# Kernel optimization log

Hardware: AMD Instinct MI355X
Metric: run time of the kernel (lower is better)

The kernel has to match this reference:

```python
import jax, jax.numpy as jnp
import numpy as np

HEADS = 12
NUM_IMS = 1
SCALE = 1.0


def _layernorm(x, g, b, eps=1e-5):
    m = jnp.mean(x, axis=-1, keepdims=True)
    v = jnp.var(x, axis=-1, keepdims=True)
    return (x - m) / jnp.sqrt(v + eps) * g + b


def _mha(q, k, v):
    # q: [B, Nq, C], k/v: [B, Nk, C]; multi-head softmax attention
    B, Nq, C = q.shape
    d = C // HEADS
    qh = q.reshape(B, Nq, HEADS, d)
    kh = k.reshape(B, k.shape[1], HEADS, d)
    vh = v.reshape(B, v.shape[1], HEADS, d)
    sim = jnp.einsum('bihd,bjhd->bhij', qh, kh) * (d ** -0.5)
    w = jax.nn.softmax(sim, axis=-1)
    out = jnp.einsum('bhij,bjhd->bihd', w, vh)
    return out.reshape(B, Nq, C)


def _forward(hidden_states, encoder_hidden_states, ln1_g, ln1_b, ln2_g, ln2_b,
             sa_wq, sa_wk, sa_wv, sa_wo, sa_wo_b, ff_ln_g, ff_ln_b, ff_w1, ff_w2,
             alpha_attn, alpha_dense, ca_wq, ca_wk, ca_wv, ca_wo, ca_wo_b):
    B, N, C = hidden_states.shape
    end_pos = encoder_hidden_states.shape[1] - 16 * NUM_IMS
    text = encoder_hidden_states[:, :end_pos]   # [B, Lt, C]
    face = encoder_hidden_states[:, end_pos:]   # [B, 16, C]

    x = hidden_states
    # gated self-attention over visual tokens + face tokens
    x_ln = _layernorm(x, ln1_g, ln1_b)
    face_ln = _layernorm(face, ln1_g, ln1_b)
    comb = jnp.concatenate([x_ln, face_ln], axis=1)  # [B, N+16, C]
    attn_out = _mha(comb @ sa_wq, comb @ sa_wk, comb @ sa_wv) @ sa_wo + sa_wo_b
    attn_out = attn_out[:, :N]
    x = x + SCALE * jnp.tanh(alpha_attn) * attn_out

    # gated GEGLU feed-forward (norm2 outside, FF has its own LayerNorm)
    h = _layernorm(x, ln2_g, ln2_b)
    h = _layernorm(h, ff_ln_g, ff_ln_b)
    h = h @ ff_w1                                 # [B, N, 2*inner]
    a, gate = jnp.split(h, 2, axis=-1)
    h = (a * jax.nn.gelu(gate, approximate=False)) @ ff_w2
    x = x + SCALE * jnp.tanh(alpha_dense) * h

    residual = x
    # cross attention against text tokens (diffusers Attention, residual_connection=True)
    out = _mha(x @ ca_wq, text @ ca_wk, text @ ca_wv) @ ca_wo + ca_wo_b
    return out + residual


def setup_inputs() -> dict:
    key = jax.random.key(0)
    ks = jax.random.split(key, 16)
    B, N, C, L, INNER = 2, 1024, 768, 77 + 16 * NUM_IMS, 3072
    W = 0.02
    return {
        'hidden_states': jax.random.normal(ks[0], (B, N, C), jnp.float32),
        'encoder_hidden_states': jax.random.normal(ks[1], (B, L, C), jnp.float32),
        'ln1_g': jnp.ones((C,), jnp.float32),
        'ln1_b': jnp.zeros((C,), jnp.float32),
        'ln2_g': jnp.ones((C,), jnp.float32),
        'ln2_b': jnp.zeros((C,), jnp.float32),
        'sa_wq': jax.random.normal(ks[2], (C, C), jnp.float32) * W,
        'sa_wk': jax.random.normal(ks[3], (C, C), jnp.float32) * W,
        'sa_wv': jax.random.normal(ks[4], (C, C), jnp.float32) * W,
        'sa_wo': jax.random.normal(ks[5], (C, C), jnp.float32) * W,
        'sa_wo_b': jnp.zeros((C,), jnp.float32),
        'ff_ln_g': jnp.ones((C,), jnp.float32),
        'ff_ln_b': jnp.zeros((C,), jnp.float32),
        'ff_w1': jax.random.normal(ks[6], (C, 2 * INNER), jnp.float32) * W,
        'ff_w2': jax.random.normal(ks[7], (INNER, C), jnp.float32) * W,
        'alpha_attn': jnp.float32(0.5),
        'alpha_dense': jnp.float32(0.5),
        'ca_wq': jax.random.normal(ks[8], (C, C), jnp.float32) * W,
        'ca_wk': jax.random.normal(ks[9], (C, C), jnp.float32) * W,
        'ca_wv': jax.random.normal(ks[10], (C, C), jnp.float32) * W,
        'ca_wo': jax.random.normal(ks[11], (C, C), jnp.float32) * W,
        'ca_wo_b': jnp.zeros((C,), jnp.float32),
    }


def reference(hidden_states, encoder_hidden_states, ln1_g, ln1_b, ln2_g, ln2_b,
              sa_wq, sa_wk, sa_wv, sa_wo, sa_wo_b, ff_ln_g, ff_ln_b, ff_w1, ff_w2,
              alpha_attn, alpha_dense, ca_wq, ca_wk, ca_wv, ca_wo, ca_wo_b):
    return _forward(hidden_states, encoder_hidden_states, ln1_g, ln1_b, ln2_g, ln2_b,
                    sa_wq, sa_wk, sa_wv, sa_wo, sa_wo_b, ff_ln_g, ff_ln_b, ff_w1, ff_w2,
                    alpha_attn, alpha_dense, ca_wq, ca_wk, ca_wv, ca_wo, ca_wo_b)
```

## Files before the change

### kernel.cpp

```cpp
#include <hip/hip_runtime.h>
#include <hip/hip_bf16.h>
#include <math.h>


#define C_DIM 768
#define B_DIM 2
#define N_DIM 1024
#define NC_DIM 1040
#define L_DIM 93
#define TEXT_LEN 77
#define INNER 3072
#define MNX 1572864

typedef unsigned short ushort_t;
typedef __bf16 bf16x8 __attribute__((ext_vector_type(8)));
typedef float f32x4 __attribute__((ext_vector_type(4)));

__device__ __forceinline__ ushort_t f2b(float f) {
  __hip_bfloat16 h = __float2bfloat16(f);
  return *(ushort_t*)&h;
}
__device__ __forceinline__ float b2f(ushort_t u) {
  __hip_bfloat16 h = *(__hip_bfloat16*)&u;
  return __bfloat162float(h);
}

__device__ __forceinline__ void g2lds16(const void* g, void* l) {
  __builtin_amdgcn_global_load_lds(
      (const __attribute__((address_space(1))) unsigned int*)g,
      (__attribute__((address_space(3))) unsigned int*)l, 16, 0, 0);
}

#define WX1    0u
#define WX2    6291456u
#define WQKV   12582912u
#define WBB1   22167552u
#define WG     47333376u
#define WS1    59916288u
#define WTEXT  63062016u
#define WATT2  63298560u
#define WWQKV  66444288u
#define WWO    69983232u
#define WW1    71162880u
#define WW2    80600064u
#define WCAWQ  85318656u
#define WCAKV  86498304u
#define WCAWO  88857600u
#define WVT1   90037248u
#define WVT2   93379584u
#define WOPART WBB1
#define WLBUF  WG
#define WATTN  (WG + 524288u)
#define WPART  WBB1

__device__ __forceinline__ float block_sum(float v, float* sh) {
#pragma unroll
  for (int o = 32; o > 0; o >>= 1) v += __shfl_down(v, o);
  int lane = threadIdx.x & 63, w = threadIdx.x >> 6;
  if (lane == 0) sh[w] = v;
  __syncthreads();
  float r = sh[0] + sh[1] + sh[2] + sh[3];
  __syncthreads();
  return r;
}

struct WtDesc {
  const float* src[10];
  ushort_t*    dst[10];
  int K[10];
  int N[10];
  int tilesX[10];
  int ileave[10];
  int start[11];
};

__global__ __launch_bounds__(256)
void wtrans_batched(WtDesc d) {
  __shared__ float tile[64][65];
  int bid = blockIdx.x;
  int j = 0;
  while (j < 9 && bid >= d.start[j + 1]) ++j;
  int ti = bid - d.start[j];
  int K = d.K[j], N = d.N[j];
  int n0 = (ti % d.tilesX[j]) * 64, k0 = (ti / d.tilesX[j]) * 64;
  const float* in = d.src[j];
  ushort_t* out = d.dst[j];
  int il = d.ileave[j];
  int t = threadIdx.x;
#pragma unroll
  for (int p = 0; p < 16; ++p) {
    int idx = t + p * 256;
    int r = idx >> 6, c = idx & 63;
    tile[r][c] = in[(size_t)(k0 + r) * N + n0 + c];
  }
  __syncthreads();
#pragma unroll
  for (int p = 0; p < 16; ++p) {
    int idx = t + p * 256;
    int r = idx >> 6, c = idx & 63;
    int nrow = n0 + r;
    int dstrow = il ? ((nrow < INNER) ? (nrow * 2) : ((nrow - INNER) * 2 + 1)) : nrow;
    out[(size_t)dstrow * K + k0 + c] = f2b(tile[c][r]);
  }
}

__global__ __launch_bounds__(256)
void ln_concat_kernel(const float* __restrict__ x, const float* __restrict__ enc,
                      const float* __restrict__ g, const float* __restrict__ b,
                      ushort_t* __restrict__ comb) {
  __shared__ float sh[4];
  int r = blockIdx.x;
  int bb = r / NC_DIM, i = r % NC_DIM;
  const float* src = (i < N_DIM)
      ? (x   + ((size_t)bb * N_DIM + i) * C_DIM)
      : (enc + ((size_t)bb * L_DIM + TEXT_LEN + (i - N_DIM)) * C_DIM);
  float v[3];
#pragma unroll
  for (int j = 0; j < 3; ++j) v[j] = src[threadIdx.x + j * 256];
  float mean = block_sum(v[0] + v[1] + v[2], sh) * (1.f / C_DIM);
  float sq = 0.f;
#pragma unroll
  for (int j = 0; j < 3; ++j) { float d = v[j] - mean; sq += d * d; }
  float rstd = rsqrtf(block_sum(sq, sh) * (1.f / C_DIM) + 1e-5f);
  ushort_t* dst = comb + (size_t)r * C_DIM;
#pragma unroll
  for (int j = 0; j < 3; ++j) {
    int c = threadIdx.x + j * 256;
    dst[c] = f2b((v[j] - mean) * rstd * g[c] + b[c]);
  }
}

__global__ __launch_bounds__(256)
void gemm_bf16(const ushort_t* __restrict__ A, const ushort_t* __restrict__ Bt,
               ushort_t* __restrict__ Ob, ushort_t* __restrict__ Og,
               int M, int N, int K) {
  __shared__ ushort_t sA[2][128 * 32];
  __shared__ ushort_t sB[2][128 * 32];
  int t = threadIdx.x;
  int w = t >> 6, ln = t & 63;
  int m0 = blockIdx.y * 128, n0 = blockIdx.x * 128;
  int wm = (w >> 1) * 64, wn = (w & 1) * 64;
  int lr = ln & 15, lq = ln >> 4;
  int seg_r = ln >> 2, seg_c = (ln & 3) * 8;

  f32x4 acc[4][4];
#pragma unroll
  for (int mi = 0; mi < 4; ++mi)
#pragma unroll
    for (int ni = 0; ni < 4; ++ni) acc[mi][ni] = (f32x4){0.f, 0.f, 0.f, 0.f};

#define STAGE(k0_, buf_)                                                     \
  do {                                                                       \
    _Pragma("unroll") for (int l = 0; l < 2; ++l) {                          \
      int s = w * 2 + l;                                                     \
      int arow = m0 + s * 16 + seg_r;                                        \
      arow = arow < M ? arow : M - 1;                                        \
      g2lds16(A + (size_t)arow * K + (k0_) + seg_c, &sA[buf_][s * 512]);     \
      int nrow = n0 + s * 16 + seg_r;                                        \
      g2lds16(Bt + (size_t)nrow * K + (k0_) + seg_c, &sB[buf_][s * 512]);    \
    }                                                                        \
  } while (0)

  STAGE(0, 0);
  __syncthreads();
  int cur = 0;
  for (int k0 = 0; k0 < K; k0 += 32) {
    if (k0 + 32 < K) STAGE(k0 + 32, cur ^ 1);
    bf16x8 af[4], bfr[4];
#pragma unroll
    for (int mi = 0; mi < 4; ++mi)
      af[mi] = *(const bf16x8*)&sA[cur][(wm + mi * 16 + lr) * 32 + lq * 8];
#pragma unroll
    for (int ni = 0; ni < 4; ++ni)
      bfr[ni] = *(const bf16x8*)&sB[cur][(wn + ni * 16 + lr) * 32 + lq * 8];
#pragma unroll
    for (int mi = 0; mi < 4; ++mi)
#pragma unroll
      for (int ni = 0; ni < 4; ++ni)
        acc[mi][ni] = __builtin_amdgcn_mfma_f32_16x16x32_bf16(
            af[mi], bfr[ni], acc[mi][ni], 0, 0, 0);
    __syncthreads();
    cur ^= 1;
  }
#undef STAGE

  if (Og) {
#pragma unroll
    for (int mi = 0; mi < 4; ++mi)
#pragma unroll
      for (int ni = 0; ni < 4; ++ni) {
        int col = n0 + wn + ni * 16 + lr;
#pragma unroll
        for (int r = 0; r < 4; ++r) {
          float val = acc[mi][ni][r];
          float other = __shfl_xor(val, 1);
          if (!(lr & 1)) {
            float a = val, gate = other;
            float ge = 0.5f * gate * (1.f + erff(gate * 0.70710678118654752f));
            int row = m0 + wm + mi * 16 + lq * 4 + r;
            Og[(size_t)row * INNER + (col >> 1)] = f2b(a * ge);
          }
        }
      }
  } else {
#pragma unroll
    for (int mi = 0; mi < 4; ++mi)
#pragma unroll
      for (int ni = 0; ni < 4; ++ni) {
        int col = n0 + wn + ni * 16 + lr;
#pragma unroll
        for (int r = 0; r < 4; ++r) {
          int row = m0 + wm + mi * 16 + lq * 4 + r;
          if (row < M) Ob[(size_t)row * N + col] = f2b(acc[mi][ni][r]);
        }
      }
  }
}

__global__ __launch_bounds__(256)
void gemm64(const ushort_t* __restrict__ A, const ushort_t* __restrict__ Bt,
            float* __restrict__ Out, ushort_t* __restrict__ Ob,
            float* __restrict__ Part,
            int M, int N, int K, int Ksplit,
            const float* __restrict__ bias, const float* __restrict__ res,
            const float* __restrict__ alphaPtr) {
  __shared__ ushort_t sA[2][4096];
  __shared__ ushort_t sB[2][4096];
  int t = threadIdx.x;
  int w = t >> 6, ln = t & 63;
  int m0 = blockIdx.y * 64, n0 = blockIdx.x * 64;
  int wm = (w >> 1) * 32, wn = (w & 1) * 32;
  int lr = ln & 15, lq = ln >> 4;
  int srow = (w & 1) * 32 + (ln >> 2);
  int skoff = (w >> 1) * 32 + (ln & 3) * 8;
  int kbeg = blockIdx.z * Ksplit;
  int kend = kbeg + Ksplit; if (kend > K) kend = K;

  f32x4 acc[2][2];
#pragma unroll
  for (int mi = 0; mi < 2; ++mi)
#pragma unroll
    for (int ni = 0; ni < 2; ++ni) acc[mi][ni] = (f32x4){0.f, 0.f, 0.f, 0.f};

#define STG64(k0_, buf_)                                                      \
  do {                                                                        \
    _Pragma("unroll") for (int i = 0; i < 2; ++i) {                           \
      int ar = m0 + srow + i * 16; ar = ar < M ? ar : M - 1;                  \
      g2lds16(A + (size_t)ar * K + (k0_) + skoff,                             \
              (char*)sA + (buf_) * 8192 + w * 2048 + i * 1024);               \
      int nr = n0 + srow + i * 16;                                            \
      g2lds16(Bt + (size_t)nr * K + (k0_) + skoff,                            \
              (char*)sB + (buf_) * 8192 + w * 2048 + i * 1024);               \
    }                                                                         \
  } while (0)

  STG64(kbeg, 0);
  __syncthreads();
  int cur = 0;
  for (int k0 = kbeg; k0 < kend; k0 += 64) {
    if (k0 + 64 < kend) STG64(k0 + 64, cur ^ 1);
#pragma unroll
    for (int s = 0; s < 2; ++s) {
      bf16x8 a0 = *(const bf16x8*)&sA[cur][s * 2048 + (wm + lr) * 32 + lq * 8];
      bf16x8 a1 = *(const bf16x8*)&sA[cur][s * 2048 + (wm + 16 + lr) * 32 + lq * 8];
      bf16x8 b0 = *(const bf16x8*)&sB[cur][s * 2048 + (wn + lr) * 32 + lq * 8];
      bf16x8 b1 = *(const bf16x8*)&sB[cur][s * 2048 + (wn + 16 + lr) * 32 + lq * 8];
      acc[0][0] = __builtin_amdgcn_mfma_f32_16x16x32_bf16(a0, b0, acc[0][0], 0, 0, 0);
      acc[0][1] = __builtin_amdgcn_mfma_f32_16x16x32_bf16(a0, b1, acc[0][1], 0, 0, 0);
      acc[1][0] = __builtin_amdgcn_mfma_f32_16x16x32_bf16(a1, b0, acc[1][0], 0, 0, 0);
      acc[1][1] = __builtin_amdgcn_mfma_f32_16x16x32_bf16(a1, b1, acc[1][1], 0, 0, 0);
    }
    __syncthreads();
    cur ^= 1;
  }
#undef STG64

  if (Part) {
    float* P = Part + (size_t)blockIdx.z * M * N;
#pragma unroll
    for (int mi = 0; mi < 2; ++mi)
#pragma unroll
      for (int ni = 0; ni < 2; ++ni) {
        int col = n0 + wn + ni * 16 + lr;
#pragma unroll
        for (int r = 0; r < 4; ++r) {
          int row = m0 + wm + mi * 16 + lq * 4 + r;
          if (row < M) P[(size_t)row * N + col] = acc[mi][ni][r];
        }
      }
  } else {
    float f = alphaPtr ? tanhf(alphaPtr[0]) : 1.0f;
#pragma unroll
    for (int mi = 0; mi < 2; ++mi)
#pragma unroll
      for (int ni = 0; ni < 2; ++ni) {
        int col = n0 + wn + ni * 16 + lr;
        float bv = bias ? bias[col] : 0.f;
#pragma unroll
        for (int r = 0; r < 4; ++r) {
          int row = m0 + wm + mi * 16 + lq * 4 + r;
          if (row < M) {
            float val = acc[mi][ni][r] + bv;
            if (res) val = res[(size_t)row * N + col] + f * val;
            if (Out) Out[(size_t)row * N + col] = val;
            if (Ob)  Ob[(size_t)row * N + col] = f2b(val);
          }
        }
      }
  }
}

__global__ __launch_bounds__(256)
void splitk_epi(const float* __restrict__ Part, int nz, float* __restrict__ Out,
                ushort_t* __restrict__ Ob, int MN, int N,
                const float* __restrict__ bias, const float* __restrict__ res,
                const float* __restrict__ alphaPtr) {
  int idx = (blockIdx.x * 256 + threadIdx.x) * 4;
  if (idx >= MN) return;
  float f = alphaPtr ? tanhf(alphaPtr[0]) : 1.0f;
  float v[4] = {0.f, 0.f, 0.f, 0.f};
  for (int z = 0; z < nz; ++z) {
    float4 a = *(const float4*)&Part[(size_t)z * MN + idx];
    v[0] += a.x; v[1] += a.y; v[2] += a.z; v[3] += a.w;
  }
  if (bias) {
    int col = idx % N;
    float4 bb = *(const float4*)&bias[col];
    v[0] += bb.x; v[1] += bb.y; v[2] += bb.z; v[3] += bb.w;
  }
  if (res) {
    float4 rr = *(const float4*)&res[idx];
    v[0] = rr.x + f * v[0]; v[1] = rr.y + f * v[1];
    v[2] = rr.z + f * v[2]; v[3] = rr.w + f * v[3];
  }
  if (Out) *(float4*)&Out[idx] = make_float4(v[0], v[1], v[2], v[3]);
  if (Ob) {
    ushort4 o;
    o.x = f2b(v[0]); o.y = f2b(v[1]); o.z = f2b(v[2]); o.w = f2b(v[3]);
    *(ushort4*)&Ob[idx] = o;
  }
}

__global__ __launch_bounds__(256)
void woepi_ln_kernel(const float* __restrict__ Part, int nz,
                     const float* __restrict__ bias, const float* __restrict__ xres,
                     const float* __restrict__ alphaPtr, float* __restrict__ x1,
                     const float* __restrict__ g1, const float* __restrict__ b1,
                     const float* __restrict__ g2, const float* __restrict__ b2,
                     ushort_t* __restrict__ hh) {
  __shared__ float sh[4];
  int row = blockIdx.x;
  float f = tanhf(alphaPtr[0]);
  float v[3];
#pragma unroll
  for (int j = 0; j < 3; ++j) {
    int c = threadIdx.x + j * 256;
    float s = 0.f;
    for (int z = 0; z < nz; ++z) s += Part[(size_t)z * MNX + (size_t)row * C_DIM + c];
    s += bias[c];
    float xv = xres[(size_t)row * C_DIM + c] + f * s;
    x1[(size_t)row * C_DIM + c] = xv;
    v[j] = xv;
  }
  float mean = block_sum(v[0] + v[1] + v[2], sh) * (1.f / C_DIM);
  float sq = 0.f;
#pragma unroll
  for (int j = 0; j < 3; ++j) { float d = v[j] - mean; sq += d * d; }
  float rstd = rsqrtf(block_sum(sq, sh) * (1.f / C_DIM) + 1e-5f);
  float y[3];
#pragma unroll
  for (int j = 0; j < 3; ++j) {
    int c = threadIdx.x + j * 256;
    y[j] = (v[j] - mean) * rstd * g1[c] + b1[c];
  }
  float mean2 = block_sum(y[0] + y[1] + y[2], sh) * (1.f / C_DIM);
  sq = 0.f;
#pragma unroll
  for (int j = 0; j < 3; ++j) { float d = y[j] - mean2; sq += d * d; }
  float rstd2 = rsqrtf(block_sum(sq, sh) * (1.f / C_DIM) + 1e-5f);
#pragma unroll
  for (int j = 0; j < 3; ++j) {
    int c = threadIdx.x + j * 256;
    hh[(size_t)row * C_DIM + c] = f2b((y[j] - mean2) * rstd2 * g2[c] + b2[c]);
  }
}

__global__ __launch_bounds__(256)
void vtrans_kernel(const ushort_t* __restrict__ V, ushort_t* __restrict__ Vt,
                   int rows_per_b, int stride, int Nk, int Nkp) {
  __shared__ ushort_t tile[64][68];
  int k0 = blockIdx.x * 64;
  int h = blockIdx.y, b = blockIdx.z;
  int t = threadIdx.x;
#pragma unroll
  for (int p = 0; p < 4; ++p) {
    int r = p * 16 + (t >> 4), c = (t & 15) * 4;
    int key = k0 + r;
    ushort4 u = make_ushort4(0, 0, 0, 0);
    if (key < Nk)
      u = *(const ushort4*)&V[((size_t)(b * rows_per_b + key)) * stride + h * 64 + c];
    *(ushort4*)&tile[r][c] = u;
  }
  __syncthreads();
  size_t base = ((size_t)(b * 12 + h)) * 64 * Nkp;
#pragma unroll
  for (int p = 0; p < 4; ++p) {
    int dv = p * 16 + (t >> 4), kc = (t & 15) * 4;
    ushort4 u;
    u.x = tile[kc + 0][dv]; u.y = tile[kc + 1][dv];
    u.z = tile[kc + 2][dv]; u.w = tile[kc + 3][dv];
    *(ushort4*)&Vt[base + (size_t)dv * Nkp + k0 + kc] = u;
  }
}

__global__ __launch_bounds__(256)
void attn_mfma(const ushort_t* __restrict__ Q, const ushort_t* __restrict__ K,
               const ushort_t* __restrict__ Vt, ushort_t* __restrict__ O,
               float* __restrict__ Opart, float* __restrict__ lbuf,
               int q_rows_per_b, int kv_rows_per_b, int Nk, int Nkp,
               int qstride, int kstride, int nchunk) {
  __shared__ ushort_t sQ[4096];
  __shared__ ushort_t sK[2][4096];
  __shared__ ushort_t sV[2][4096];
  __shared__ ushort_t sP[4][1024];
  const float scale = 0.18033688011112042f;
  const float M0 = 16.0f;
  int t = threadIdx.x;
  int w = t >> 6, ln = t & 63;
  int col = ln & 15, quad = ln >> 4;
  int z = blockIdx.z;
  int b = z / nchunk, kc = z % nchunk;
  int h = blockIdx.y, q0 = blockIdx.x * 64;
  size_t vt_base = ((size_t)(b * 12 + h)) * 64 * Nkp;
  int ntiles = Nkp >> 6;
  int t0 = (kc * ntiles) / nchunk;
  int t1 = ((kc + 1) * ntiles) / nchunk;

#define STAGE_KV(kt_, bb_)                                                    \
  do {                                                                        \
    _Pragma("unroll") for (int s = 0; s < 2; ++s) {                           \
      int key = (kt_) * 64 + w * 16 + (ln >> 2);                              \
      g2lds16(K + (size_t)(b * kv_rows_per_b + key) * kstride                 \
                + h * 64 + s * 32 + (ln & 3) * 8,                             \
              (char*)sK[bb_] + s * 4096 + w * 1024);                          \
      int dv = w * 16 + (ln >> 2);                                            \
      g2lds16(Vt + vt_base + (size_t)dv * Nkp                                 \
                + (kt_) * 64 + s * 32 + (ln & 3) * 8,                         \
              (char*)sV[bb_] + s * 4096 + w * 1024);                          \
    }                                                                         \
  } while (0)

#pragma unroll
  for (int s = 0; s < 2; ++s) {
    int r = q0 + w * 16 + (ln >> 2);
    g2lds16(Q + (size_t)(b * q_rows_per_b + r) * qstride + h * 64 + s * 32 + (ln & 3) * 8,
            (char*)sQ + s * 4096 + w * 1024);
  }
  STAGE_KV(t0, 0);
  __syncthreads();
  bf16x8 qa[2];
#pragma unroll
  for (int s = 0; s < 2; ++s)
    qa[s] = *(const bf16x8*)&sQ[s * 2048 + (w * 16 + col) * 32 + quad * 8];

  f32x4 oacc[4];
#pragma unroll
  for (int i = 0; i < 4; ++i) oacc[i] = (f32x4){0.f, 0.f, 0.f, 0.f};
  float l_i[4] = {0.f, 0.f, 0.f, 0.f};

  ushort_t* sPw = sP[w];
  int bb = 0;

  for (int kt = t0; kt < t1; ++kt) {
    if (kt + 1 < t1) STAGE_KV(kt + 1, bb ^ 1);

    f32x4 cs[4];
#pragma unroll
    for (int nblk = 0; nblk < 4; ++nblk) {
      cs[nblk] = (f32x4){0.f, 0.f, 0.f, 0.f};
#pragma unroll
      for (int s = 0; s < 2; ++s) {
        bf16x8 kb = *(const bf16x8*)&sK[bb][s * 2048 + (nblk * 16 + col) * 32 + quad * 8];
        cs[nblk] = __builtin_amdgcn_mfma_f32_16x16x32_bf16(qa[s], kb, cs[nblk], 0, 0, 0);
      }
    }
    if (kt * 64 + 64 > Nk) {
#pragma unroll
      for (int nblk = 0; nblk < 4; ++nblk) {
        bool valid = (kt * 64 + nblk * 16 + col) < Nk;
#pragma unroll
        for (int r = 0; r < 4; ++r)
          cs[nblk][r] = valid ? cs[nblk][r] : -1e30f;
      }
    }
#pragma unroll
    for (int r = 0; r < 4; ++r) {
      int row = quad * 4 + r;
#pragma unroll
      for (int nblk = 0; nblk < 4; ++nblk) {
        float p = exp2f(fmaf(cs[nblk][r], scale, -M0));
        l_i[r] += p;
        int kin = (nblk & 1) * 16 + col;
        sPw[(nblk >> 1) * 512 + row * 32 + (kin ^ (quad << 3))] = f2b(p);
      }
    }
#pragma unroll
    for (int s = 0; s < 2; ++s) {
      bf16x8 pa = *(const bf16x8*)&sPw[s * 512 + col * 32 + ((quad ^ ((col >> 2) & 3)) << 3)];
#pragma unroll
      for (int nblk = 0; nblk < 4; ++nblk) {
        bf16x8 vb = *(const bf16x8*)&sV[bb][s * 2048 + (nblk * 16 + col) * 32 + quad * 8];
        oacc[nblk] = __builtin_amdgcn_mfma_f32_16x16x32_bf16(pa, vb, oacc[nblk], 0, 0, 0);
      }
    }
    if (kt + 1 < t1) __syncthreads();
    bb ^= 1;
  }
#undef STAGE_KV

#pragma unroll
  for (int r = 0; r < 4; ++r) {
    float ps = l_i[r];
#pragma unroll
    for (int o = 1; o < 16; o <<= 1) ps += __shfl_xor(ps, o);
    int qglob = b * N_DIM + q0 + w * 16 + quad * 4 + r;
    if (Opart) {
      if (col == 0) lbuf[(size_t)kc * (B_DIM * N_DIM * 12) + (size_t)qglob * 12 + h] = ps;
      float* op = Opart + (size_t)kc * MNX + (size_t)qglob * C_DIM + h * 64;
#pragma unroll
      for (int nblk = 0; nblk < 4; ++nblk)
        op[nblk * 16 + col] = oacc[nblk][r];
    } else {
      float inv = 1.f / ps;
#pragma unroll
      for (int nblk = 0; nblk < 4; ++nblk)
        O[(size_t)qglob * C_DIM + h * 64 + nblk * 16 + col] = f2b(oacc[nblk][r] * inv);
    }
  }
}

__global__ __launch_bounds__(256)
void attn_merge(const float* __restrict__ Opart, const float* __restrict__ lbuf,
                ushort_t* __restrict__ Ob, int nchunk) {
  int idx = (blockIdx.x * 256 + threadIdx.x) * 4;
  if (idx >= MNX) return;
  int row = idx / C_DIM, c = idx % C_DIM;
  int h = c >> 6;
  float l = 0.f;
  float v[4] = {0.f, 0.f, 0.f, 0.f};
  for (int kc = 0; kc < nchunk; ++kc) {
    l += lbuf[(size_t)kc * (B_DIM * N_DIM * 12) + (size_t)row * 12 + h];
    float4 p = *(const float4*)&Opart[(size_t)kc * MNX + idx];
    v[0] += p.x; v[1] += p.y; v[2] += p.z; v[3] += p.w;
  }
  float inv = 1.f / l;
  ushort4 o;
  o.x = f2b(v[0] * inv); o.y = f2b(v[1] * inv);
  o.z = f2b(v[2] * inv); o.w = f2b(v[3] * inv);
  *(ushort4*)&Ob[idx] = o;
}

__global__ __launch_bounds__(256)
void gather_text_kernel(const float* __restrict__ enc, ushort_t* __restrict__ out) {
  int r = blockIdx.x;
  int bb = r / TEXT_LEN, j = r % TEXT_LEN;
  const float* src = enc + ((size_t)bb * L_DIM + j) * C_DIM;
  ushort_t* dst = out + (size_t)r * C_DIM;
#pragma unroll
  for (int l = 0; l < 3; ++l) {
    int c = threadIdx.x + l * 256;
    dst[c] = f2b(src[c]);
  }
}

extern "C" void kernel_launch(void* const* d_in, const int* in_sizes, int n_in,
                              void* d_out, int out_size, void* d_ws, size_t ws_size,
                              hipStream_t stream) {
  const float* x        = (const float*)d_in[0];
  const float* enc      = (const float*)d_in[1];
  const float* ln1_g    = (const float*)d_in[2];
  const float* ln1_b    = (const float*)d_in[3];
  const float* ln2_g    = (const float*)d_in[4];
  const float* ln2_b    = (const float*)d_in[5];
  const float* sa_wq    = (const float*)d_in[6];
  const float* sa_wk    = (const float*)d_in[7];
  const float* sa_wv    = (const float*)d_in[8];
  const float* sa_wo    = (const float*)d_in[9];
  const float* sa_wo_b  = (const float*)d_in[10];
  const float* ff_ln_g  = (const float*)d_in[11];
  const float* ff_ln_b  = (const float*)d_in[12];
  const float* ff_w1    = (const float*)d_in[13];
  const float* ff_w2    = (const float*)d_in[14];
  const float* a_attn   = (const float*)d_in[15];
  const float* a_dense  = (const float*)d_in[16];
  const float* ca_wq    = (const float*)d_in[17];
  const float* ca_wk    = (const float*)d_in[18];
  const float* ca_wv    = (const float*)d_in[19];
  const float* ca_wo    = (const float*)d_in[20];
  const float* ca_wo_b  = (const float*)d_in[21];

  char* ws = (char*)d_ws;
  float*    x1     = (float*)(ws + WX1);
  float*    x2     = (float*)(ws + WX2);
  ushort_t* qkv_b  = (ushort_t*)(ws + WQKV);
  ushort_t* q2b    = (ushort_t*)(ws + WQKV);
  ushort_t* kv2b   = (ushort_t*)(ws + WQKV + 3145728u);
  ushort_t* comb_b = (ushort_t*)(ws + WBB1);
  float*    opart  = (float*)(ws + WOPART);
  float*    lbuf   = (float*)(ws + WLBUF);
  ushort_t* attn_b = (ushort_t*)(ws + WATTN);
  ushort_t* g_b    = (ushort_t*)(ws + WG);
  ushort_t* hh     = (ushort_t*)(ws + WS1);
  ushort_t* x2b    = (ushort_t*)(ws + WS1);
  ushort_t* text_b = (ushort_t*)(ws + WTEXT);
  ushort_t* attn2b = (ushort_t*)(ws + WATT2);
  ushort_t* wqkv_t = (ushort_t*)(ws + WWQKV);
  ushort_t* wo_t   = (ushort_t*)(ws + WWO);
  ushort_t* w1_t   = (ushort_t*)(ws + WW1);
  ushort_t* w2_t   = (ushort_t*)(ws + WW2);
  ushort_t* cawq_t = (ushort_t*)(ws + WCAWQ);
  ushort_t* cakv_t = (ushort_t*)(ws + WCAKV);
  ushort_t* cawo_t = (ushort_t*)(ws + WCAWO);
  ushort_t* vt1    = (ushort_t*)(ws + WVT1);
  ushort_t* vt2    = (ushort_t*)(ws + WVT2);
  float* part = (float*)(ws + WPART);
  float* out = (float*)d_out;

  const int Mc = B_DIM * NC_DIM;
  const int Mx = B_DIM * N_DIM;
  const int Mt = B_DIM * TEXT_LEN;

  WtDesc wd;
  const float* srcs[10] = {sa_wq, sa_wk, sa_wv, sa_wo, ca_wq, ca_wk, ca_wv, ca_wo, ff_w1, ff_w2};
  ushort_t* dsts[10] = {wqkv_t, wqkv_t + 589824, wqkv_t + 2 * 589824, wo_t,
                        cawq_t, cakv_t, cakv_t + 589824, cawo_t, w1_t, w2_t};
  int Ks[10] = {768, 768, 768, 768, 768, 768, 768, 768, 768, 3072};
  int Ns[10] = {768, 768, 768, 768, 768, 768, 768, 768, 6144, 768};
  int total = 0;
  for (int j = 0; j < 10; ++j) {
    wd.src[j] = srcs[j]; wd.dst[j] = dsts[j];
    wd.K[j] = Ks[j]; wd.N[j] = Ns[j];
    wd.tilesX[j] = Ns[j] / 64;
    wd.ileave[j] = (j == 8) ? 1 : 0;
    wd.start[j] = total;
    total += (Ns[j] / 64) * (Ks[j] / 64);
  }
  wd.start[10] = total;

  wtrans_batched<<<total, 256, 0, stream>>>(wd);
  ln_concat_kernel<<<Mc, 256, 0, stream>>>(x, enc, ln1_g, ln1_b, comb_b);
  gemm64<<<dim3(36, 33, 1), 256, 0, stream>>>(
      comb_b, wqkv_t, nullptr, qkv_b, nullptr, Mc, 2304, 768, 768,
      nullptr, nullptr, nullptr);
  vtrans_kernel<<<dim3(17, 12, B_DIM), 256, 0, stream>>>(
      qkv_b + 1536, vt1, NC_DIM, 2304, NC_DIM, 1088);
  attn_mfma<<<dim3(N_DIM / 64, 12, B_DIM * 4), 256, 0, stream>>>(
      qkv_b + 0, qkv_b + 768, vt1, nullptr, opart, lbuf,
      NC_DIM, NC_DIM, NC_DIM, 1088, 2304, 2304, 4);
  attn_merge<<<MNX / 1024, 256, 0, stream>>>(opart, lbuf, attn_b, 4);
  gemm64<<<dim3(12, 32, 2), 256, 0, stream>>>(
      attn_b, wo_t, nullptr, nullptr, part, Mx, 768, 768, 384,
      nullptr, nullptr, nullptr);
  woepi_ln_kernel<<<Mx, 256, 0, stream>>>(
      part, 2, sa_wo_b, x, a_attn, x1, ln2_g, ln2_b, ff_ln_g, ff_ln_b, hh);
  gemm_bf16<<<dim3(48, 16), 256, 0, stream>>>(
      hh, w1_t, nullptr, g_b, Mx, 6144, 768);
  gemm64<<<dim3(12, 32, 4), 256, 0, stream>>>(
      g_b, w2_t, nullptr, nullptr, part, Mx, 768, 3072, 768,
      nullptr, nullptr, nullptr);
  splitk_epi<<<MNX / 1024, 256, 0, stream>>>(
      part, 4, x2, x2b, MNX, 768, nullptr, x1, a_dense);
  gather_text_kernel<<<Mt, 256, 0, stream>>>(enc, text_b);
  gemm64<<<dim3(12, 32, 2), 256, 0, stream>>>(
      x2b, cawq_t, nullptr, nullptr, part, Mx, 768, 768, 384,
      nullptr, nullptr, nullptr);
  splitk_epi<<<MNX / 1024, 256, 0, stream>>>(
      part, 2, nullptr, q2b, MNX, 768, nullptr, nullptr, nullptr);
  gemm64<<<dim3(24, 3, 1), 256, 0, stream>>>(
      text_b, cakv_t, nullptr, kv2b, nullptr, Mt, 1536, 768, 768,
      nullptr, nullptr, nullptr);
  vtrans_kernel<<<dim3(2, 12, B_DIM), 256, 0, stream>>>(
      kv2b + 768, vt2, TEXT_LEN, 1536, TEXT_LEN, 128);
  attn_mfma<<<dim3(N_DIM / 64, 12, B_DIM), 256, 0, stream>>>(
      q2b, kv2b + 0, vt2, attn2b, nullptr, nullptr,
      N_DIM, TEXT_LEN, TEXT_LEN, 128, 768, 1536, 1);
  gemm64<<<dim3(12, 32, 2), 256, 0, stream>>>(
      attn2b, cawo_t, nullptr, nullptr, part, Mx, 768, 768, 384,
      nullptr, nullptr, nullptr);
  splitk_epi<<<MNX / 1024, 256, 0, stream>>>(
      part, 2, out, nullptr, MNX, 768, ca_wo_b, x2, nullptr);
}
```

Before: 325.3 us.

## Drop split-K on 768-wide GEMMs, fuse epilogues, use gemm64 for GEGLU FF1

The three 768x768 projections no longer use split-K. Their bias, gated residual and bf16 output now happen in the gemm64 epilogue, which removes the partial-buffer writes and the extra splitk_epi launches. The woepi_ln kernel becomes a plain double-LayerNorm kernel that reads x1 written by the fused GEMM. The FF1 GEGLU GEMM moves from the 128x128 gemm_bf16 kernel to the 64x64 gemm64 kernel with a GEGLU epilogue, which gives more blocks but less reuse per block. Dropping split-K leaves 384 blocks with a longer K loop for the 768-wide GEMMs, so parallelism goes down.

```diff
diff --git a/kernel.cpp b/kernel.cpp
--- a/kernel.cpp
+++ b/kernel.cpp
@@ -131,96 +131,43 @@
 }
 
 __global__ __launch_bounds__(256)
-void gemm_bf16(const ushort_t* __restrict__ A, const ushort_t* __restrict__ Bt,
-               ushort_t* __restrict__ Ob, ushort_t* __restrict__ Og,
-               int M, int N, int K) {
-  __shared__ ushort_t sA[2][128 * 32];
-  __shared__ ushort_t sB[2][128 * 32];
-  int t = threadIdx.x;
-  int w = t >> 6, ln = t & 63;
-  int m0 = blockIdx.y * 128, n0 = blockIdx.x * 128;
-  int wm = (w >> 1) * 64, wn = (w & 1) * 64;
-  int lr = ln & 15, lq = ln >> 4;
-  int seg_r = ln >> 2, seg_c = (ln & 3) * 8;
-
-  f32x4 acc[4][4];
-#pragma unroll
-  for (int mi = 0; mi < 4; ++mi)
-#pragma unroll
-    for (int ni = 0; ni < 4; ++ni) acc[mi][ni] = (f32x4){0.f, 0.f, 0.f, 0.f};
-
-#define STAGE(k0_, buf_)                                                     \
-  do {                                                                       \
-    _Pragma("unroll") for (int l = 0; l < 2; ++l) {                          \
-      int s = w * 2 + l;                                                     \
-      int arow = m0 + s * 16 + seg_r;                                        \
-      arow = arow < M ? arow : M - 1;                                        \
-      g2lds16(A + (size_t)arow * K + (k0_) + seg_c, &sA[buf_][s * 512]);     \
-      int nrow = n0 + s * 16 + seg_r;                                        \
-      g2lds16(Bt + (size_t)nrow * K + (k0_) + seg_c, &sB[buf_][s * 512]);    \
-    }                                                                        \
-  } while (0)
-
-  STAGE(0, 0);
-  __syncthreads();
-  int cur = 0;
-  for (int k0 = 0; k0 < K; k0 += 32) {
-    if (k0 + 32 < K) STAGE(k0 + 32, cur ^ 1);
-    bf16x8 af[4], bfr[4];
-#pragma unroll
-    for (int mi = 0; mi < 4; ++mi)
-      af[mi] = *(const bf16x8*)&sA[cur][(wm + mi * 16 + lr) * 32 + lq * 8];
-#pragma unroll
-    for (int ni = 0; ni < 4; ++ni)
-      bfr[ni] = *(const bf16x8*)&sB[cur][(wn + ni * 16 + lr) * 32 + lq * 8];
-#pragma unroll
-    for (int mi = 0; mi < 4; ++mi)
-#pragma unroll
-      for (int ni = 0; ni < 4; ++ni)
-        acc[mi][ni] = __builtin_amdgcn_mfma_f32_16x16x32_bf16(
-            af[mi], bfr[ni], acc[mi][ni], 0, 0, 0);
-    __syncthreads();
-    cur ^= 1;
-  }
-#undef STAGE
-
-  if (Og) {
-#pragma unroll
-    for (int mi = 0; mi < 4; ++mi)
-#pragma unroll
-      for (int ni = 0; ni < 4; ++ni) {
-        int col = n0 + wn + ni * 16 + lr;
-#pragma unroll
-        for (int r = 0; r < 4; ++r) {
-          float val = acc[mi][ni][r];
-          float other = __shfl_xor(val, 1);
-          if (!(lr & 1)) {
-            float a = val, gate = other;
-            float ge = 0.5f * gate * (1.f + erff(gate * 0.70710678118654752f));
-            int row = m0 + wm + mi * 16 + lq * 4 + r;
-            Og[(size_t)row * INNER + (col >> 1)] = f2b(a * ge);
-          }
-        }
-      }
-  } else {
-#pragma unroll
-    for (int mi = 0; mi < 4; ++mi)
-#pragma unroll
-      for (int ni = 0; ni < 4; ++ni) {
-        int col = n0 + wn + ni * 16 + lr;
-#pragma unroll
-        for (int r = 0; r < 4; ++r) {
-          int row = m0 + wm + mi * 16 + lq * 4 + r;
-          if (row < M) Ob[(size_t)row * N + col] = f2b(acc[mi][ni][r]);
-        }
-      }
+void ln_double_kernel(const float* __restrict__ src,
+                      const float* __restrict__ g1, const float* __restrict__ b1,
+                      const float* __restrict__ g2, const float* __restrict__ b2,
+                      ushort_t* __restrict__ out) {
+  __shared__ float sh[4];
+  const float* s = src + (size_t)blockIdx.x * C_DIM;
+  float v[3];
+#pragma unroll
+  for (int j = 0; j < 3; ++j) v[j] = s[threadIdx.x + j * 256];
+  float mean = block_sum(v[0] + v[1] + v[2], sh) * (1.f / C_DIM);
+  float sq = 0.f;
+#pragma unroll
+  for (int j = 0; j < 3; ++j) { float d = v[j] - mean; sq += d * d; }
+  float rstd = rsqrtf(block_sum(sq, sh) * (1.f / C_DIM) + 1e-5f);
+  float y[3];
+#pragma unroll
+  for (int j = 0; j < 3; ++j) {
+    int c = threadIdx.x + j * 256;
+    y[j] = (v[j] - mean) * rstd * g1[c] + b1[c];
+  }
+  float mean2 = block_sum(y[0] + y[1] + y[2], sh) * (1.f / C_DIM);
+  sq = 0.f;
+#pragma unroll
+  for (int j = 0; j < 3; ++j) { float d = y[j] - mean2; sq += d * d; }
+  float rstd2 = rsqrtf(block_sum(sq, sh) * (1.f / C_DIM) + 1e-5f);
+  ushort_t* dst = out + (size_t)blockIdx.x * C_DIM;
+#pragma unroll
+  for (int j = 0; j < 3; ++j) {
+    int c = threadIdx.x + j * 256;
+    dst[c] = f2b((y[j] - mean2) * rstd2 * g2[c] + b2[c]);
   }
 }
 
 __global__ __launch_bounds__(256)
 void gemm64(const ushort_t* __restrict__ A, const ushort_t* __restrict__ Bt,
             float* __restrict__ Out, ushort_t* __restrict__ Ob,
-            float* __restrict__ Part,
+            ushort_t* __restrict__ Og, float* __restrict__ Part,
             int M, int N, int K, int Ksplit,
             const float* __restrict__ bias, const float* __restrict__ res,
             const float* __restrict__ alphaPtr) {
@@ -275,7 +222,25 @@
   }
 #undef STG64
 
-  if (Part) {
+  if (Og) {
+#pragma unroll
+    for (int mi = 0; mi < 2; ++mi)
+#pragma unroll
+      for (int ni = 0; ni < 2; ++ni) {
+        int col = n0 + wn + ni * 16 + lr;
+#pragma unroll
+        for (int r = 0; r < 4; ++r) {
+          float val = acc[mi][ni][r];
+          float other = __shfl_xor(val, 1);
+          if (!(lr & 1)) {
+            float a = val, gate = other;
+            float ge = 0.5f * gate * (1.f + erff(gate * 0.70710678118654752f));
+            int row = m0 + wm + mi * 16 + lq * 4 + r;
+            if (row < M) Og[(size_t)row * INNER + (col >> 1)] = f2b(a * ge);
+          }
+        }
+      }
+  } else if (Part) {
     float* P = Part + (size_t)blockIdx.z * M * N;
 #pragma unroll
     for (int mi = 0; mi < 2; ++mi)
@@ -338,50 +303,6 @@
     ushort4 o;
     o.x = f2b(v[0]); o.y = f2b(v[1]); o.z = f2b(v[2]); o.w = f2b(v[3]);
     *(ushort4*)&Ob[idx] = o;
-  }
-}
-
-__global__ __launch_bounds__(256)
-void woepi_ln_kernel(const float* __restrict__ Part, int nz,
-                     const float* __restrict__ bias, const float* __restrict__ xres,
-                     const float* __restrict__ alphaPtr, float* __restrict__ x1,
-                     const float* __restrict__ g1, const float* __restrict__ b1,
-                     const float* __restrict__ g2, const float* __restrict__ b2,
-                     ushort_t* __restrict__ hh) {
-  __shared__ float sh[4];
-  int row = blockIdx.x;
-  float f = tanhf(alphaPtr[0]);
-  float v[3];
-#pragma unroll
-  for (int j = 0; j < 3; ++j) {
-    int c = threadIdx.x + j * 256;
-    float s = 0.f;
-    for (int z = 0; z < nz; ++z) s += Part[(size_t)z * MNX + (size_t)row * C_DIM + c];
-    s += bias[c];
-    float xv = xres[(size_t)row * C_DIM + c] + f * s;
-    x1[(size_t)row * C_DIM + c] = xv;
-    v[j] = xv;
-  }
-  float mean = block_sum(v[0] + v[1] + v[2], sh) * (1.f / C_DIM);
-  float sq = 0.f;
-#pragma unroll
-  for (int j = 0; j < 3; ++j) { float d = v[j] - mean; sq += d * d; }
-  float rstd = rsqrtf(block_sum(sq, sh) * (1.f / C_DIM) + 1e-5f);
-  float y[3];
-#pragma unroll
-  for (int j = 0; j < 3; ++j) {
-    int c = threadIdx.x + j * 256;
-    y[j] = (v[j] - mean) * rstd * g1[c] + b1[c];
-  }
-  float mean2 = block_sum(y[0] + y[1] + y[2], sh) * (1.f / C_DIM);
-  sq = 0.f;
-#pragma unroll
-  for (int j = 0; j < 3; ++j) { float d = y[j] - mean2; sq += d * d; }
-  float rstd2 = rsqrtf(block_sum(sq, sh) * (1.f / C_DIM) + 1e-5f);
-#pragma unroll
-  for (int j = 0; j < 3; ++j) {
-    int c = threadIdx.x + j * 256;
-    hh[(size_t)row * C_DIM + c] = f2b((y[j] - mean2) * rstd2 * g2[c] + b2[c]);
   }
 }
 
@@ -650,7 +571,7 @@
   wtrans_batched<<<total, 256, 0, stream>>>(wd);
   ln_concat_kernel<<<Mc, 256, 0, stream>>>(x, enc, ln1_g, ln1_b, comb_b);
   gemm64<<<dim3(36, 33, 1), 256, 0, stream>>>(
-      comb_b, wqkv_t, nullptr, qkv_b, nullptr, Mc, 2304, 768, 768,
+      comb_b, wqkv_t, nullptr, qkv_b, nullptr, nullptr, Mc, 2304, 768, 768,
       nullptr, nullptr, nullptr);
   vtrans_kernel<<<dim3(17, 12, B_DIM), 256, 0, stream>>>(
       qkv_b + 1536, vt1, NC_DIM, 2304, NC_DIM, 1088);
@@ -658,35 +579,31 @@
       qkv_b + 0, qkv_b + 768, vt1, nullptr, opart, lbuf,
       NC_DIM, NC_DIM, NC_DIM, 1088, 2304, 2304, 4);
   attn_merge<<<MNX / 1024, 256, 0, stream>>>(opart, lbuf, attn_b, 4);
-  gemm64<<<dim3(12, 32, 2), 256, 0, stream>>>(
-      attn_b, wo_t, nullptr, nullptr, part, Mx, 768, 768, 384,
+  gemm64<<<dim3(12, 32, 1), 256, 0, stream>>>(
+      attn_b, wo_t, x1, nullptr, nullptr, nullptr, Mx, 768, 768, 768,
+      sa_wo_b, x, a_attn);
+  ln_double_kernel<<<Mx, 256, 0, stream>>>(x1, ln2_g, ln2_b, ff_ln_g, ff_ln_b, hh);
+  gemm64<<<dim3(96, 32, 1), 256, 0, stream>>>(
+      hh, w1_t, nullptr, nullptr, g_b, nullptr, Mx, 6144, 768, 768,
       nullptr, nullptr, nullptr);
-  woepi_ln_kernel<<<Mx, 256, 0, stream>>>(
-      part, 2, sa_wo_b, x, a_attn, x1, ln2_g, ln2_b, ff_ln_g, ff_ln_b, hh);
-  gemm_bf16<<<dim3(48, 16), 256, 0, stream>>>(
-      hh, w1_t, nullptr, g_b, Mx, 6144, 768);
   gemm64<<<dim3(12, 32, 4), 256, 0, stream>>>(
-      g_b, w2_t, nullptr, nullptr, part, Mx, 768, 3072, 768,
+      g_b, w2_t, nullptr, nullptr, nullptr, part, Mx, 768, 3072, 768,
       nullptr, nullptr, nullptr);
   splitk_epi<<<MNX / 1024, 256, 0, stream>>>(
       part, 4, x2, x2b, MNX, 768, nullptr, x1, a_dense);
   gather_text_kernel<<<Mt, 256, 0, stream>>>(enc, text_b);
-  gemm64<<<dim3(12, 32, 2), 256, 0, stream>>>(
-      x2b, cawq_t, nullptr, nullptr, part, Mx, 768, 768, 384,
+  gemm64<<<dim3(12, 32, 1), 256, 0, stream>>>(
+      x2b, cawq_t, nullptr, q2b, nullptr, nullptr, Mx, 768, 768, 768,
       nullptr, nullptr, nullptr);
-  splitk_epi<<<MNX / 1024, 256, 0, stream>>>(
-      part, 2, nullptr, q2b, MNX, 768, nullptr, nullptr, nullptr);
   gemm64<<<dim3(24, 3, 1), 256, 0, stream>>>(
-      text_b, cakv_t, nullptr, kv2b, nullptr, Mt, 1536, 768, 768,
+      text_b, cakv_t, nullptr, kv2b, nullptr, nullptr, Mt, 1536, 768, 768,
       nullptr, nullptr, nullptr);
   vtrans_kernel<<<dim3(2, 12, B_DIM), 256, 0, stream>>>(
       kv2b + 768, vt2, TEXT_LEN, 1536, TEXT_LEN, 128);
   attn_mfma<<<dim3(N_DIM / 64, 12, B_DIM), 256, 0, stream>>>(
       q2b, kv2b + 0, vt2, attn2b, nullptr, nullptr,
       N_DIM, TEXT_LEN, TEXT_LEN, 128, 768, 1536, 1);
-  gemm64<<<dim3(12, 32, 2), 256, 0, stream>>>(
-      attn2b, cawo_t, nullptr, nullptr, part, Mx, 768, 768, 384,
-      nullptr, nullptr, nullptr);
-  splitk_epi<<<MNX / 1024, 256, 0, stream>>>(
-      part, 2, out, nullptr, MNX, 768, ca_wo_b, x2, nullptr);
-}
+  gemm64<<<dim3(12, 32, 1), 256, 0, stream>>>(
+      attn2b, cawo_t, out, nullptr, nullptr, nullptr, Mx, 768, 768, 768,
+      ca_wo_b, x2, nullptr);
+}
```

Measured after the change: 336.4 us. 1.03x slower.
